# Kernel optimization log

Measured on AMD Instinct MI355X. Metric: run time of the kernel, lower is better.

## Reference

```python
import jax, jax.numpy as jnp
import numpy as np

N_NODES = 50000
N_EDGES = 640000
HID = 128
EDGE_FEAT = 4
NUM_G = 20
R_MIN, R_MAX = 0.0, 10.0

def setup_inputs() -> dict:
    key = jax.random.key(0)
    ks = jax.random.split(key, 16)
    s = lambda d: 1.0 / np.sqrt(d)
    return {
        'h': jax.random.normal(ks[0], (N_NODES, HID), jnp.float32),
        'x': jax.random.normal(ks[1], (N_NODES, 3), jnp.float32),
        'edge_index': jax.random.randint(ks[2], (2, N_EDGES), 0, N_NODES, dtype=jnp.int64),
        'mask_ligand': jnp.ones((N_NODES,), jnp.float32),
        'edge_attr': jax.random.normal(ks[3], (N_EDGES, EDGE_FEAT), jnp.float32),
        'We1': jax.random.normal(ks[4], (2*HID+EDGE_FEAT+NUM_G, HID), jnp.float32) * s(2*HID+EDGE_FEAT+NUM_G),
        'be1': jnp.zeros((HID,), jnp.float32),
        'We2': jax.random.normal(ks[5], (HID, HID), jnp.float32) * s(HID),
        'be2': jnp.zeros((HID,), jnp.float32),
        'Winf': jax.random.normal(ks[6], (HID, 1), jnp.float32) * s(HID),
        'binf': jnp.zeros((1,), jnp.float32),
        'Wx1': jax.random.normal(ks[7], (HID, HID), jnp.float32) * s(HID),
        'bx1': jnp.zeros((HID,), jnp.float32),
        'Wx2': jax.random.normal(ks[8], (HID, 1), jnp.float32) * 0.001 * s(HID),
        'Wn1': jax.random.normal(ks[9], (2*HID, HID), jnp.float32) * s(2*HID),
        'bn1': jnp.zeros((HID,), jnp.float32),
        'Wn2': jax.random.normal(ks[10], (HID, HID), jnp.float32) * s(HID),
        'bn2': jnp.zeros((HID,), jnp.float32),
    }

def reference(h, x, edge_index, mask_ligand, edge_attr,
              We1, be1, We2, be2, Winf, binf, Wx1, bx1, Wx2, Wn1, bn1, Wn2, bn2):
    n = h.shape[0]
    src, dst = edge_index[0], edge_index[1]
    hi, hj = h[dst], h[src]                      # [E, H] gathers
    rel_x = x[dst] - x[src]                      # [E, 3]
    d_sq = jnp.sum(rel_x**2, axis=-1, keepdims=True)  # [E, 1]
    d = jnp.sqrt(d_sq + 1e-8)
    # GaussianSmearing(r_min=0, r_max=10, num_gaussians=20)
    offset = jnp.linspace(R_MIN, R_MAX, NUM_G, dtype=h.dtype)
    coeff = -0.5 / (offset[1] - offset[0])**2
    d_feat = jnp.exp(coeff * (d - offset)**2)    # [E, 20]
    edge_feat = jnp.concatenate([d_feat, edge_attr], axis=-1)
    # edge MLP (2 layers, silu, act_last=True)
    z = jnp.concatenate([hi, hj, edge_feat], axis=-1)
    mij = jax.nn.silu(jax.nn.silu(z @ We1 + be1) @ We2 + be2)  # [E, H]
    eij = jax.nn.sigmoid(mij @ Winf + binf)      # [E, 1]
    mi = jax.ops.segment_sum(mij * eij, dst, num_segments=n)   # [N, H]
    # node MLP (2 layers, silu, no act on last)
    nz = jnp.concatenate([mi, h], axis=-1)
    h_out = h + (jax.nn.silu(nz @ Wn1 + bn1) @ Wn2 + bn2)
    # coordinate update
    xg = jnp.tanh(jax.nn.silu(mij @ Wx1 + bx1) @ Wx2)          # [E, 1]
    delta_x = jax.ops.segment_sum(rel_x / (d + 1.0) * xg, dst, num_segments=n)
    x_out = x + delta_x * mask_ligand[:, None]
    return h_out, x_out
```

## Files before the change

kernel.cpp:

```cpp
#include <hip/hip_runtime.h>
#include <math.h>

#define NN 50000
#define NE 640000
#define H 128
#define EPB 32
#define NPB 32
#define ZB 296
#define BB 136
#define KP1 288
#define NZB 264
#define NBPAD 50176
#define HISTB (NE / 256)
#define CONVB 464
#define ALLOCB (NBPAD / 256)
#define HCONVB 3125

typedef __attribute__((ext_vector_type(8))) unsigned short u16x8;
typedef __attribute__((ext_vector_type(8))) __bf16 bf16x8;
typedef __attribute__((ext_vector_type(2))) __bf16 bf16x2;
typedef __attribute__((ext_vector_type(4))) float f32x4;

__device__ __forceinline__ float frcp(float x) {
#if __has_builtin(__builtin_amdgcn_rcpf)
    return __builtin_amdgcn_rcpf(x);
#else
    return 1.0f / x;
#endif
}

__device__ __forceinline__ float silu_f(float v) {
    return v * frcp(1.0f + __expf(-v));
}

__device__ __forceinline__ float sigmoid_f(float v) {
    return frcp(1.0f + __expf(-v));
}

__device__ __forceinline__ float tanh_f(float v) {
    return 1.0f - 2.0f * frcp(1.0f + __expf(2.0f * v));
}

__device__ __forceinline__ unsigned short f2bf(float f) {
    unsigned int u = __builtin_bit_cast(unsigned int, f);
    u += 0x7FFFu + ((u >> 16) & 1u);
    return (unsigned short)(u >> 16);
}

__device__ __forceinline__ float bf2f(unsigned short s) {
    unsigned int u = ((unsigned int)s) << 16;
    return __builtin_bit_cast(float, u);
}

__device__ __forceinline__ unsigned int pkbf(float lo, float hi) {
#if __has_builtin(__builtin_amdgcn_cvt_pk_bf16_f32)
    bf16x2 v = __builtin_amdgcn_cvt_pk_bf16_f32(lo, hi);
    unsigned int r; __builtin_memcpy(&r, &v, 4); return r;
#else
    return (unsigned int)f2bf(lo) | ((unsigned int)f2bf(hi) << 16);
#endif
}

__device__ __forceinline__ f32x4 mfma16(u16x8 a, u16x8 b, f32x4 c) {
    return __builtin_amdgcn_mfma_f32_16x16x32_bf16(
        __builtin_bit_cast(bf16x8, a), __builtin_bit_cast(bf16x8, b), c, 0, 0, 0);
}

template<int KT, int INSTR, bool SYNC_BEFORE_EPI>
__device__ __forceinline__ void layer_mfma(
    const unsigned short* __restrict__ inbuf,
    const unsigned short* __restrict__ wt,
    const float* __restrict__ bias,
    unsigned short* __restrict__ outbuf,
    int wv, int quad, int r16)
{
    f32x4 acc[2][2] = {};
    const int F = wv * 32;
    #pragma unroll
    for (int ks = 0; ks < KT / 32; ks++) {
        int ko = ks * 32 + quad * 8;
        u16x8 b0 = *(const u16x8*)(inbuf + r16 * INSTR + ko);
        u16x8 b1 = *(const u16x8*)(inbuf + (16 + r16) * INSTR + ko);
        u16x8 a0 = *(const u16x8*)(wt + (size_t)(F + r16) * KT + ko);
        u16x8 a1 = *(const u16x8*)(wt + (size_t)(F + 16 + r16) * KT + ko);
        acc[0][0] = mfma16(a0, b0, acc[0][0]);
        acc[0][1] = mfma16(a0, b1, acc[0][1]);
        acc[1][0] = mfma16(a1, b0, acc[1][0]);
        acc[1][1] = mfma16(a1, b1, acc[1][1]);
    }
    if (SYNC_BEFORE_EPI) __syncthreads();
    #pragma unroll
    for (int rt = 0; rt < 2; rt++) {
        int f0 = F + rt * 16 + quad * 4;
        float4 bv = *(const float4*)(bias + f0);
        #pragma unroll
        for (int ci = 0; ci < 2; ci++) {
            int e = ci * 16 + r16;
            float s0 = silu_f(acc[rt][ci][0] + bv.x);
            float s1 = silu_f(acc[rt][ci][1] + bv.y);
            float s2 = silu_f(acc[rt][ci][2] + bv.z);
            float s3 = silu_f(acc[rt][ci][3] + bv.w);
            uint2 p = { pkbf(s0, s1), pkbf(s2, s3) };
            *(uint2*)(outbuf + e * BB + f0) = p;
        }
    }
}

__global__ __launch_bounds__(256) void init_kernel(
    float4* __restrict__ out4, int n4out,
    float4* __restrict__ ws4, int n4ws)
{
    int i = blockIdx.x * 256 + threadIdx.x;
    float4 z = make_float4(0.f, 0.f, 0.f, 0.f);
    if (i < n4out) out4[i] = z;
    else if (i - n4out < n4ws) ws4[i - n4out] = z;
}

__global__ __launch_bounds__(256) void hist_conv_kernel(
    const int* __restrict__ ei, int* __restrict__ cnt, int histBlocks,
    const float* __restrict__ We1, const float* __restrict__ We2,
    const float* __restrict__ Wx1, const float* __restrict__ Wn1,
    const float* __restrict__ Wn2,
    unsigned short* __restrict__ w1t, unsigned short* __restrict__ w2t,
    unsigned short* __restrict__ wx1t, unsigned short* __restrict__ wn1t,
    unsigned short* __restrict__ wn2t)
{
    int b = blockIdx.x, t = threadIdx.x;
    if (b < histBlocks) {
        int i = b * 256 + t;
        atomicAdd(&cnt[ei[NE + i]], 1);
        return;
    }
    int i = (b - histBlocks) * 256 + t;
    const int S1 = 128 * KP1;
    const int S2 = 128 * 128;
    const int S3 = 128 * 256;
    if (i < S1) {
        int n = i / KP1, k = i % KP1;
        w1t[i] = (k < 280) ? f2bf(We1[k * H + n]) : (unsigned short)0;
    } else if (i < S1 + S2) {
        int j = i - S1; int n = j / H, k = j % H;
        w2t[j] = f2bf(We2[k * H + n]);
    } else if (i < S1 + 2 * S2) {
        int j = i - S1 - S2; int n = j / H, k = j % H;
        wx1t[j] = f2bf(Wx1[k * H + n]);
    } else if (i < S1 + 2 * S2 + S3) {
        int j = i - S1 - 2 * S2; int n = j / 256, k = j % 256;
        wn1t[j] = f2bf(Wn1[k * H + n]);
    } else if (i < S1 + 3 * S2 + S3) {
        int j = i - S1 - 2 * S2 - S3; int n = j / H, k = j % H;
        wn2t[j] = f2bf(Wn2[k * H + n]);
    }
}

__global__ __launch_bounds__(256) void alloc_hconv_kernel(
    const int* __restrict__ cnt, int* __restrict__ cur, int* __restrict__ gtot,
    const float* __restrict__ h, unsigned short* __restrict__ hb,
    int allocBlocks)
{
    int b = blockIdx.x, t = threadIdx.x;
    if (b < allocBlocks) {
        int d = b * 256 + t;
        int v = cnt[d];
        int incl = v;
        #pragma unroll
        for (int o = 1; o < 64; o <<= 1) {
            int u = __shfl_up(incl, o, 64);
            if ((t & 63) >= o) incl += u;
        }
        int total = __shfl(incl, 63, 64);
        int base = 0;
        if ((t & 63) == 63) base = atomicAdd(gtot, total);
        base = __shfl(base, 63, 64);
        cur[d] = base + incl - v;
        return;
    }
    int j = (b - allocBlocks) * 256 + t;
    const float4* hp = (const float4*)h + (size_t)j * 2;
    float4 a = hp[0], c = hp[1];
    uint4 pk = { pkbf(a.x, a.y), pkbf(a.z, a.w), pkbf(c.x, c.y), pkbf(c.z, c.w) };
    ((uint4*)hb)[j] = pk;
}

__global__ __launch_bounds__(256) void scatter_kernel(
    const int* __restrict__ ei, const float* __restrict__ edge_attr,
    int* __restrict__ cur, uint4* __restrict__ epay)
{
    int i = blockIdx.x * 256 + threadIdx.x;
    int s = ei[i], d = ei[NE + i];
    float4 ea = ((const float4*)edge_attr)[i];
    int p = atomicAdd(&cur[d], 1);
    uint4 pv = { (unsigned)s, (unsigned)d, pkbf(ea.x, ea.y), pkbf(ea.z, ea.w) };
    epay[p] = pv;
}

__global__ __launch_bounds__(256, 7) void edge_kernel(
    const float* __restrict__ h, const float* __restrict__ x,
    const int* __restrict__ ei, const float* __restrict__ edge_attr,
    const unsigned short* __restrict__ w1t, const float* __restrict__ be1,
    const unsigned short* __restrict__ w2t, const float* __restrict__ be2,
    const float* __restrict__ Winf, const float* __restrict__ binf,
    const unsigned short* __restrict__ wx1t, const float* __restrict__ bx1,
    const float* __restrict__ Wx2,
    const uint4* __restrict__ epay, const unsigned short* __restrict__ hb,
    float* __restrict__ mi, float* __restrict__ dx)
{
    __shared__ unsigned short zs[EPB * ZB];
    __shared__ float relx_s[EPB][3];
    __shared__ float eij_s[EPB];
    __shared__ float epart[4][EPB];
    __shared__ float xpart[4][EPB];
    __shared__ int dst_s[EPB];
    __shared__ float winf_s[H];
    __shared__ float wx2_s[H];

    unsigned short* m1 = zs;
    unsigned short* m2 = zs + EPB * BB;

    const int t = threadIdx.x;
    const int e0 = blockIdx.x * EPB;
    const bool srt = (epay != nullptr);

    if (t >= 128 && t < 256) {
        winf_s[t - 128] = Winf[t - 128];
        wx2_s[t - 128] = Wx2[t - 128];
    }

    {
        int e = t >> 3, l = t & 7;
        unsigned short* zr = zs + e * ZB;
        if (srt) {
            uint4 pv = epay[e0 + e];
            const uint4* hd = (const uint4*)(hb + (size_t)pv.y * H);
            const uint4* hs = (const uint4*)(hb + (size_t)pv.x * H);
            uint4 a0 = hd[l * 2], a1 = hd[l * 2 + 1];
            *(uint4*)(zr + l * 16) = a0;
            *(uint4*)(zr + l * 16 + 8) = a1;
            uint4 c0 = hs[l * 2], c1 = hs[l * 2 + 1];
            *(uint4*)(zr + 128 + l * 16) = c0;
            *(uint4*)(zr + 128 + l * 16 + 8) = c1;
        } else {
            int s = ei[e0 + e], d = ei[NE + e0 + e];
            const float4* hd = (const float4*)(h + (size_t)d * H);
            const float4* hs = (const float4*)(h + (size_t)s * H);
            float4 v0 = hd[l * 4 + 0], v1 = hd[l * 4 + 1];
            float4 v2 = hd[l * 4 + 2], v3 = hd[l * 4 + 3];
            uint4 p0 = { pkbf(v0.x, v0.y), pkbf(v0.z, v0.w), pkbf(v1.x, v1.y), pkbf(v1.z, v1.w) };
            uint4 p1 = { pkbf(v2.x, v2.y), pkbf(v2.z, v2.w), pkbf(v3.x, v3.y), pkbf(v3.z, v3.w) };
            *(uint4*)(zr + l * 16) = p0;
            *(uint4*)(zr + l * 16 + 8) = p1;
            float4 w0 = hs[l * 4 + 0], w1 = hs[l * 4 + 1];
            float4 w2 = hs[l * 4 + 2], w3 = hs[l * 4 + 3];
            uint4 q0 = { pkbf(w0.x, w0.y), pkbf(w0.z, w0.w), pkbf(w1.x, w1.y), pkbf(w1.z, w1.w) };
            uint4 q1 = { pkbf(w2.x, w2.y), pkbf(w2.z, w2.w), pkbf(w3.x, w3.y), pkbf(w3.z, w3.w) };
            *(uint4*)(zr + 128 + l * 16) = q0;
            *(uint4*)(zr + 128 + l * 16 + 8) = q1;
        }
    }
    if (t < EPB) {
        unsigned short* zr = zs + t * ZB;
        int s, d;
        if (srt) {
            uint4 pv = epay[e0 + t];
            s = (int)pv.x; d = (int)pv.y;
            *(unsigned int*)(zr + 276) = pv.z;
            *(unsigned int*)(zr + 278) = pv.w;
        } else {
            s = ei[e0 + t]; d = ei[NE + e0 + t];
            #pragma unroll
            for (int j = 0; j < 4; j++)
                zr[276 + j] = f2bf(edge_attr[(size_t)(e0 + t) * 4 + j]);
        }
        dst_s[t] = d;
        float rx = x[d * 3 + 0] - x[s * 3 + 0];
        float ry = x[d * 3 + 1] - x[s * 3 + 1];
        float rz = x[d * 3 + 2] - x[s * 3 + 2];
        float d2 = rx * rx + ry * ry + rz * rz;
        float dd = sqrtf(d2 + 1e-8f);
        float inv = frcp(dd + 1.0f);
        relx_s[t][0] = rx * inv;
        relx_s[t][1] = ry * inv;
        relx_s[t][2] = rz * inv;
        const float step = 10.0f / 19.0f;
        const float coeff = -0.5f / (step * step);
        #pragma unroll
        for (int g = 0; g < 20; g++) {
            float df = dd - step * (float)g;
            zr[256 + g] = f2bf(__expf(coeff * df * df));
        }
        #pragma unroll
        for (int j = 280; j < ZB; j++) zr[j] = 0;
    }
    __syncthreads();

    const int wv = t >> 6, lane = t & 63;
    const int quad = lane >> 4, r16 = lane & 15;
    const int F = wv * 32;

    layer_mfma<KP1, ZB, true>(zs, w1t, be1, m1, wv, quad, r16);
    __syncthreads();

    {
        f32x4 acc[2][2] = {};
        #pragma unroll
        for (int ks = 0; ks < H / 32; ks++) {
            int ko = ks * 32 + quad * 8;
            u16x8 b0 = *(const u16x8*)(m1 + r16 * BB + ko);
            u16x8 b1 = *(const u16x8*)(m1 + (16 + r16) * BB + ko);
            u16x8 a0 = *(const u16x8*)(w2t + (size_t)(F + r16) * H + ko);
            u16x8 a1 = *(const u16x8*)(w2t + (size_t)(F + 16 + r16) * H + ko);
            acc[0][0] = mfma16(a0, b0, acc[0][0]);
            acc[0][1] = mfma16(a0, b1, acc[0][1]);
            acc[1][0] = mfma16(a1, b0, acc[1][0]);
            acc[1][1] = mfma16(a1, b1, acc[1][1]);
        }
        float ep[2] = {0.f, 0.f};
        #pragma unroll
        for (int rt = 0; rt < 2; rt++) {
            int f0 = F + rt * 16 + quad * 4;
            float4 bv = *(const float4*)(be2 + f0);
            float4 wf = *(const float4*)(winf_s + f0);
            #pragma unroll
            for (int ci = 0; ci < 2; ci++) {
                int e = ci * 16 + r16;
                float s0 = silu_f(acc[rt][ci][0] + bv.x);
                float s1 = silu_f(acc[rt][ci][1] + bv.y);
                float s2 = silu_f(acc[rt][ci][2] + bv.z);
                float s3 = silu_f(acc[rt][ci][3] + bv.w);
                ep[ci] += s0 * wf.x + s1 * wf.y + s2 * wf.z + s3 * wf.w;
                uint2 p = { pkbf(s0, s1), pkbf(s2, s3) };
                *(uint2*)(m2 + e * BB + f0) = p;
            }
        }
        #pragma unroll
        for (int ci = 0; ci < 2; ci++) {
            ep[ci] += __shfl_xor(ep[ci], 16, 64);
            ep[ci] += __shfl_xor(ep[ci], 32, 64);
        }
        if (quad == 0) {
            epart[wv][r16] = ep[0];
            epart[wv][16 + r16] = ep[1];
        }
    }
    __syncthreads();

    if (t < EPB) {
        float s = epart[0][t] + epart[1][t] + epart[2][t] + epart[3][t] + binf[0];
        eij_s[t] = sigmoid_f(s);
    }

    {
        f32x4 acc[2][2] = {};
        #pragma unroll
        for (int ks = 0; ks < H / 32; ks++) {
            int ko = ks * 32 + quad * 8;
            u16x8 b0 = *(const u16x8*)(m2 + r16 * BB + ko);
            u16x8 b1 = *(const u16x8*)(m2 + (16 + r16) * BB + ko);
            u16x8 a0 = *(const u16x8*)(wx1t + (size_t)(F + r16) * H + ko);
            u16x8 a1 = *(const u16x8*)(wx1t + (size_t)(F + 16 + r16) * H + ko);
            acc[0][0] = mfma16(a0, b0, acc[0][0]);
            acc[0][1] = mfma16(a0, b1, acc[0][1]);
            acc[1][0] = mfma16(a1, b0, acc[1][0]);
            acc[1][1] = mfma16(a1, b1, acc[1][1]);
        }
        float xp[2] = {0.f, 0.f};
        #pragma unroll
        for (int rt = 0; rt < 2; rt++) {
            int f0 = F + rt * 16 + quad * 4;
            float4 bv = *(const float4*)(bx1 + f0);
            float4 wf = *(const float4*)(wx2_s + f0);
            #pragma unroll
            for (int ci = 0; ci < 2; ci++) {
                xp[ci] += silu_f(acc[rt][ci][0] + bv.x) * wf.x
                        + silu_f(acc[rt][ci][1] + bv.y) * wf.y
                        + silu_f(acc[rt][ci][2] + bv.z) * wf.z
                        + silu_f(acc[rt][ci][3] + bv.w) * wf.w;
            }
        }
        #pragma unroll
        for (int ci = 0; ci < 2; ci++) {
            xp[ci] += __shfl_xor(xp[ci], 16, 64);
            xp[ci] += __shfl_xor(xp[ci], 32, 64);
        }
        if (quad == 0) {
            xpart[wv][r16] = xp[0];
            xpart[wv][16 + r16] = xp[1];
        }
    }
    __syncthreads();

    {
        if (t < 128) {
            const int k = t;
            float acc = 0.f;
            int rs = 0;
            #pragma unroll 1
            for (int e = 0; e < EPB; e++) {
                acc += bf2f(m2[e * BB + k]) * eij_s[e];
                if (e == EPB - 1 || dst_s[e + 1] != dst_s[e]) {
                    float* p = &mi[(size_t)dst_s[e] * H + k];
                    if (srt && rs > 0 && e < EPB - 1) *p = acc;
                    else atomicAdd(p, acc);
                    acc = 0.f;
                    rs = e + 1;
                }
            }
        } else if (t < 131) {
            const int dd = t - 128;
            float acc = 0.f;
            #pragma unroll 1
            for (int e = 0; e < EPB; e++) {
                float xs = xpart[0][e] + xpart[1][e] + xpart[2][e] + xpart[3][e];
                acc += relx_s[e][dd] * tanh_f(xs);
                if (e == EPB - 1 || dst_s[e + 1] != dst_s[e]) {
                    atomicAdd(&dx[(size_t)dst_s[e] * 3 + dd], acc);
                    acc = 0.f;
                }
            }
        }
    }
}

__global__ __launch_bounds__(256, 8) void node_kernel(
    const float* __restrict__ h, const float* __restrict__ x,
    const float* __restrict__ mask,
    const unsigned short* __restrict__ wn1t, const float* __restrict__ bn1,
    const unsigned short* __restrict__ wn2t, const float* __restrict__ bn2,
    float* __restrict__ mi_hout, float* __restrict__ dx_xout)
{
    __shared__ unsigned short nzs[NPB * NZB];

    unsigned short* nbuf = nzs;

    const int t = threadIdx.x;
    const int n0 = blockIdx.x * NPB;

    {
        int r = t >> 3, l = t & 7;
        int n = n0 + r;
        unsigned short* zr = nzs + r * NZB;
        if (n < NN) {
            const float4* mi4 = (const float4*)(mi_hout + (size_t)n * H);
            const float4* h4  = (const float4*)(h + (size_t)n * H);
            float4 v0 = mi4[l * 4 + 0], v1 = mi4[l * 4 + 1];
            float4 v2 = mi4[l * 4 + 2], v3 = mi4[l * 4 + 3];
            uint4 p0 = { pkbf(v0.x, v0.y), pkbf(v0.z, v0.w), pkbf(v1.x, v1.y), pkbf(v1.z, v1.w) };
            uint4 p1 = { pkbf(v2.x, v2.y), pkbf(v2.z, v2.w), pkbf(v3.x, v3.y), pkbf(v3.z, v3.w) };
            *(uint4*)(zr + l * 16) = p0;
            *(uint4*)(zr + l * 16 + 8) = p1;
            float4 w0 = h4[l * 4 + 0], w1 = h4[l * 4 + 1];
            float4 w2 = h4[l * 4 + 2], w3 = h4[l * 4 + 3];
            uint4 q0 = { pkbf(w0.x, w0.y), pkbf(w0.z, w0.w), pkbf(w1.x, w1.y), pkbf(w1.z, w1.w) };
            uint4 q1 = { pkbf(w2.x, w2.y), pkbf(w2.z, w2.w), pkbf(w3.x, w3.y), pkbf(w3.z, w3.w) };
            *(uint4*)(zr + 128 + l * 16) = q0;
            *(uint4*)(zr + 128 + l * 16 + 8) = q1;
        } else {
            uint4 zf = {0u, 0u, 0u, 0u};
            *(uint4*)(zr + l * 16) = zf;
            *(uint4*)(zr + l * 16 + 8) = zf;
            *(uint4*)(zr + 128 + l * 16) = zf;
            *(uint4*)(zr + 128 + l * 16 + 8) = zf;
        }
    }

    float xo = 0.f;
    int xn = -1, xdim = 0;
    if (t < NPB * 3) {
        int r = t / 3; xdim = t % 3;
        int n = n0 + r;
        if (n < NN) {
            xn = n;
            xo = x[(size_t)n * 3 + xdim] + dx_xout[(size_t)n * 3 + xdim] * mask[n];
        }
    }
    __syncthreads();

    if (xn >= 0) dx_xout[(size_t)xn * 3 + xdim] = xo;

    const int wv = t >> 6, lane = t & 63;
    const int quad = lane >> 4, r16 = lane & 15;

    layer_mfma<2 * H, NZB, true>(nzs, wn1t, bn1, nbuf, wv, quad, r16);
    __syncthreads();

    {
        f32x4 acc[2][2] = {};
        const int F = wv * 32;
        #pragma unroll
        for (int ks = 0; ks < H / 32; ks++) {
            int ko = ks * 32 + quad * 8;
            u16x8 b0 = *(const u16x8*)(nbuf + r16 * BB + ko);
            u16x8 b1 = *(const u16x8*)(nbuf + (16 + r16) * BB + ko);
            u16x8 a0 = *(const u16x8*)(wn2t + (size_t)(F + r16) * H + ko);
            u16x8 a1 = *(const u16x8*)(wn2t + (size_t)(F + 16 + r16) * H + ko);
            acc[0][0] = mfma16(a0, b0, acc[0][0]);
            acc[0][1] = mfma16(a0, b1, acc[0][1]);
            acc[1][0] = mfma16(a1, b0, acc[1][0]);
            acc[1][1] = mfma16(a1, b1, acc[1][1]);
        }
        #pragma unroll
        for (int rt = 0; rt < 2; rt++) {
            int f0 = F + rt * 16 + quad * 4;
            float4 bv = *(const float4*)(bn2 + f0);
            #pragma unroll
            for (int ci = 0; ci < 2; ci++) {
                int n = n0 + ci * 16 + r16;
                if (n < NN) {
                    float4 hv = *(const float4*)(h + (size_t)n * H + f0);
                    float4 o;
                    o.x = hv.x + acc[rt][ci][0] + bv.x;
                    o.y = hv.y + acc[rt][ci][1] + bv.y;
                    o.z = hv.z + acc[rt][ci][2] + bv.z;
                    o.w = hv.w + acc[rt][ci][3] + bv.w;
                    *(float4*)(mi_hout + (size_t)n * H + f0) = o;
                }
            }
        }
    }
}

extern "C" void kernel_launch(void* const* d_in, const int* in_sizes, int n_in,
                              void* d_out, int out_size, void* d_ws, size_t ws_size,
                              hipStream_t stream) {
    const float* h     = (const float*)d_in[0];
    const float* x     = (const float*)d_in[1];
    const int*   ei    = (const int*)d_in[2];
    const float* mask  = (const float*)d_in[3];
    const float* eattr = (const float*)d_in[4];
    const float* We1   = (const float*)d_in[5];
    const float* be1   = (const float*)d_in[6];
    const float* We2   = (const float*)d_in[7];
    const float* be2   = (const float*)d_in[8];
    const float* Winf  = (const float*)d_in[9];
    const float* binf  = (const float*)d_in[10];
    const float* Wx1   = (const float*)d_in[11];
    const float* bx1   = (const float*)d_in[12];
    const float* Wx2   = (const float*)d_in[13];
    const float* Wn1   = (const float*)d_in[14];
    const float* bn1   = (const float*)d_in[15];
    const float* Wn2   = (const float*)d_in[16];
    const float* bn2   = (const float*)d_in[17];

    float* mi = (float*)d_out;
    float* dx = mi + (size_t)NN * H;

    char* wsb  = (char*)d_ws;
    unsigned short* w1t  = (unsigned short*)wsb;
    unsigned short* w2t  = w1t + 128 * KP1;
    unsigned short* wx1t = w2t + 128 * H;
    unsigned short* wn1t = wx1t + 128 * H;
    unsigned short* wn2t = wn1t + 128 * 256;

    const size_t OFF_CNT  = 262144;
    const size_t OFF_CUR  = OFF_CNT + (size_t)NBPAD * 4;
    const size_t OFF_GTOT = OFF_CUR + (size_t)NBPAD * 4;
    const size_t OFF_HB   = OFF_GTOT + 16;
    const size_t OFF_EPAY = OFF_HB + (size_t)NN * H * 2;
    const size_t WS_NEED  = OFF_EPAY + (size_t)NE * 16;

    int*   cnt  = (int*)(wsb + OFF_CNT);
    int*   cur  = (int*)(wsb + OFF_CUR);
    int*   gtot = (int*)(wsb + OFF_GTOT);
    unsigned short* hb = (unsigned short*)(wsb + OFF_HB);
    uint4* epay = (uint4*)(wsb + OFF_EPAY);

    const bool full = (ws_size >= WS_NEED);

    const int n4out = (NN * H + NN * 3) / 4;
    const int n4ws  = full ? (int)((OFF_HB - OFF_CNT) / 16) : 0;
    init_kernel<<<(n4out + n4ws + 255) / 256, 256, 0, stream>>>(
        (float4*)d_out, n4out, (float4*)(wsb + OFF_CNT), n4ws);

    {
        int hb_ = full ? HISTB : 0;
        hist_conv_kernel<<<hb_ + CONVB, 256, 0, stream>>>(
            ei, cnt, hb_, We1, We2, Wx1, Wn1, Wn2, w1t, w2t, wx1t, wn1t, wn2t);
    }

    if (full) {
        alloc_hconv_kernel<<<ALLOCB + HCONVB, 256, 0, stream>>>(
            cnt, cur, gtot, h, hb, ALLOCB);
        scatter_kernel<<<NE / 256, 256, 0, stream>>>(ei, eattr, cur, epay);
    }

    edge_kernel<<<NE / EPB, 256, 0, stream>>>(
        h, x, ei, eattr, w1t, be1, w2t, be2, Winf, binf, wx1t, bx1, Wx2,
        full ? epay : (const uint4*)nullptr,
        full ? hb : (const unsigned short*)nullptr,
        mi, dx);

    node_kernel<<<(NN + NPB - 1) / NPB, 256, 0, stream>>>(
        h, x, mask, wn1t, bn1, wn2t, bn2, mi, dx);
}
```

Before: 511.7 us.

## Double edge tile to 64 edges with 512-thread blocks and reuse weight fragments

```diff
diff --git a/kernel.cpp b/kernel.cpp
--- a/kernel.cpp
+++ b/kernel.cpp
@@ -4,7 +4,7 @@
 #define NN 50000
 #define NE 640000
 #define H 128
-#define EPB 32
+#define EPB 64
 #define NPB 32
 #define ZB 296
 #define BB 136
@@ -194,7 +194,7 @@
     epay[p] = pv;
 }
 
-__global__ __launch_bounds__(256, 7) void edge_kernel(
+__global__ __launch_bounds__(512, 6) void edge_kernel(
     const float* __restrict__ h, const float* __restrict__ x,
     const int* __restrict__ ei, const float* __restrict__ edge_attr,
     const unsigned short* __restrict__ w1t, const float* __restrict__ be1,
@@ -208,8 +208,9 @@
     __shared__ unsigned short zs[EPB * ZB];
     __shared__ float relx_s[EPB][3];
     __shared__ float eij_s[EPB];
-    __shared__ float epart[4][EPB];
-    __shared__ float xpart[4][EPB];
+    __shared__ float xg_s[EPB];
+    __shared__ float epart[8][EPB];
+    __shared__ float xpart[8][EPB];
     __shared__ int dst_s[EPB];
     __shared__ float winf_s[H];
     __shared__ float wx2_s[H];
@@ -295,108 +296,139 @@
 
     const int wv = t >> 6, lane = t & 63;
     const int quad = lane >> 4, r16 = lane & 15;
-    const int F = wv * 32;
-
-    layer_mfma<KP1, ZB, true>(zs, w1t, be1, m1, wv, quad, r16);
+    const int F = wv * 16;
+    const int f0 = F + quad * 4;
+
+    {
+        f32x4 acc[4] = {};
+        #pragma unroll
+        for (int ks = 0; ks < KP1 / 32; ks++) {
+            int ko = ks * 32 + quad * 8;
+            u16x8 a = *(const u16x8*)(w1t + (size_t)(F + r16) * KP1 + ko);
+            #pragma unroll
+            for (int ci = 0; ci < 4; ci++) {
+                u16x8 b = *(const u16x8*)(zs + (ci * 16 + r16) * ZB + ko);
+                acc[ci] = mfma16(a, b, acc[ci]);
+            }
+        }
+        __syncthreads();
+        float4 bv = *(const float4*)(be1 + f0);
+        #pragma unroll
+        for (int ci = 0; ci < 4; ci++) {
+            int e = ci * 16 + r16;
+            float s0 = silu_f(acc[ci][0] + bv.x);
+            float s1 = silu_f(acc[ci][1] + bv.y);
+            float s2 = silu_f(acc[ci][2] + bv.z);
+            float s3 = silu_f(acc[ci][3] + bv.w);
+            uint2 p = { pkbf(s0, s1), pkbf(s2, s3) };
+            *(uint2*)(m1 + e * BB + f0) = p;
+        }
+    }
     __syncthreads();
 
     {
-        f32x4 acc[2][2] = {};
+        f32x4 acc[4] = {};
         #pragma unroll
         for (int ks = 0; ks < H / 32; ks++) {
             int ko = ks * 32 + quad * 8;
-            u16x8 b0 = *(const u16x8*)(m1 + r16 * BB + ko);
-            u16x8 b1 = *(const u16x8*)(m1 + (16 + r16) * BB + ko);
-            u16x8 a0 = *(const u16x8*)(w2t + (size_t)(F + r16) * H + ko);
-            u16x8 a1 = *(const u16x8*)(w2t + (size_t)(F + 16 + r16) * H + ko);
-            acc[0][0] = mfma16(a0, b0, acc[0][0]);
-            acc[0][1] = mfma16(a0, b1, acc[0][1]);
-            acc[1][0] = mfma16(a1, b0, acc[1][0]);
-            acc[1][1] = mfma16(a1, b1, acc[1][1]);
-        }
-        float ep[2] = {0.f, 0.f};
-        #pragma unroll
-        for (int rt = 0; rt < 2; rt++) {
-            int f0 = F + rt * 16 + quad * 4;
-            float4 bv = *(const float4*)(be2 + f0);
-            float4 wf = *(const float4*)(winf_s + f0);
-            #pragma unroll
-            for (int ci = 0; ci < 2; ci++) {
-                int e = ci * 16 + r16;
-                float s0 = silu_f(acc[rt][ci][0] + bv.x);
-                float s1 = silu_f(acc[rt][ci][1] + bv.y);
-                float s2 = silu_f(acc[rt][ci][2] + bv.z);
-                float s3 = silu_f(acc[rt][ci][3] + bv.w);
-                ep[ci] += s0 * wf.x + s1 * wf.y + s2 * wf.z + s3 * wf.w;
-                uint2 p = { pkbf(s0, s1), pkbf(s2, s3) };
-                *(uint2*)(m2 + e * BB + f0) = p;
+            u16x8 a = *(const u16x8*)(w2t + (size_t)(F + r16) * H + ko);
+            #pragma unroll
+            for (int ci = 0; ci < 4; ci++) {
+                u16x8 b = *(const u16x8*)(m1 + (ci * 16 + r16) * BB + ko);
+                acc[ci] = mfma16(a, b, acc[ci]);
             }
         }
-        #pragma unroll
-        for (int ci = 0; ci < 2; ci++) {
+        float4 bv = *(const float4*)(be2 + f0);
+        float4 wf = *(const float4*)(winf_s + f0);
+        float ep[4];
+        #pragma unroll
+        for (int ci = 0; ci < 4; ci++) {
+            int e = ci * 16 + r16;
+            float s0 = silu_f(acc[ci][0] + bv.x);
+            float s1 = silu_f(acc[ci][1] + bv.y);
+            float s2 = silu_f(acc[ci][2] + bv.z);
+            float s3 = silu_f(acc[ci][3] + bv.w);
+            ep[ci] = s0 * wf.x + s1 * wf.y + s2 * wf.z + s3 * wf.w;
+            uint2 p = { pkbf(s0, s1), pkbf(s2, s3) };
+            *(uint2*)(m2 + e * BB + f0) = p;
+        }
+        #pragma unroll
+        for (int ci = 0; ci < 4; ci++) {
             ep[ci] += __shfl_xor(ep[ci], 16, 64);
             ep[ci] += __shfl_xor(ep[ci], 32, 64);
         }
         if (quad == 0) {
-            epart[wv][r16] = ep[0];
-            epart[wv][16 + r16] = ep[1];
+            #pragma unroll
+            for (int ci = 0; ci < 4; ci++)
+                epart[wv][ci * 16 + r16] = ep[ci];
         }
     }
     __syncthreads();
 
     if (t < EPB) {
-        float s = epart[0][t] + epart[1][t] + epart[2][t] + epart[3][t] + binf[0];
+        float s = binf[0];
+        #pragma unroll
+        for (int w = 0; w < 8; w++) s += epart[w][t];
         eij_s[t] = sigmoid_f(s);
     }
 
     {
-        f32x4 acc[2][2] = {};
+        f32x4 acc[4] = {};
         #pragma unroll
         for (int ks = 0; ks < H / 32; ks++) {
             int ko = ks * 32 + quad * 8;
-            u16x8 b0 = *(const u16x8*)(m2 + r16 * BB + ko);
-            u16x8 b1 = *(const u16x8*)(m2 + (16 + r16) * BB + ko);
-            u16x8 a0 = *(const u16x8*)(wx1t + (size_t)(F + r16) * H + ko);
-            u16x8 a1 = *(const u16x8*)(wx1t + (size_t)(F + 16 + r16) * H + ko);
-            acc[0][0] = mfma16(a0, b0, acc[0][0]);
-            acc[0][1] = mfma16(a0, b1, acc[0][1]);
-            acc[1][0] = mfma16(a1, b0, acc[1][0]);
-            acc[1][1] = mfma16(a1, b1, acc[1][1]);
-        }
-        float xp[2] = {0.f, 0.f};
-        #pragma unroll
-        for (int rt = 0; rt < 2; rt++) {
-            int f0 = F + rt * 16 + quad * 4;
-            float4 bv = *(const float4*)(bx1 + f0);
-            float4 wf = *(const float4*)(wx2_s + f0);
-            #pragma unroll
-            for (int ci = 0; ci < 2; ci++) {
-                xp[ci] += silu_f(acc[rt][ci][0] + bv.x) * wf.x
-                        + silu_f(acc[rt][ci][1] + bv.y) * wf.y
-                        + silu_f(acc[rt][ci][2] + bv.z) * wf.z
-                        + silu_f(acc[rt][ci][3] + bv.w) * wf.w;
+            u16x8 a = *(const u16x8*)(wx1t + (size_t)(F + r16) * H + ko);
+            #pragma unroll
+            for (int ci = 0; ci < 4; ci++) {
+                u16x8 b = *(const u16x8*)(m2 + (ci * 16 + r16) * BB + ko);
+                acc[ci] = mfma16(a, b, acc[ci]);
             }
         }
-        #pragma unroll
-        for (int ci = 0; ci < 2; ci++) {
+        float4 bv = *(const float4*)(bx1 + f0);
+        float4 wf = *(const float4*)(wx2_s + f0);
+        float xp[4];
+        #pragma unroll
+        for (int ci = 0; ci < 4; ci++) {
+            xp[ci] = silu_f(acc[ci][0] + bv.x) * wf.x
+                   + silu_f(acc[ci][1] + bv.y) * wf.y
+                   + silu_f(acc[ci][2] + bv.z) * wf.z
+                   + silu_f(acc[ci][3] + bv.w) * wf.w;
+        }
+        #pragma unroll
+        for (int ci = 0; ci < 4; ci++) {
             xp[ci] += __shfl_xor(xp[ci], 16, 64);
             xp[ci] += __shfl_xor(xp[ci], 32, 64);
         }
         if (quad == 0) {
-            xpart[wv][r16] = xp[0];
-            xpart[wv][16 + r16] = xp[1];
+            #pragma unroll
+            for (int ci = 0; ci < 4; ci++)
+                xpart[wv][ci * 16 + r16] = xp[ci];
         }
     }
     __syncthreads();
 
-    {
-        if (t < 128) {
-            const int k = t;
-            float acc = 0.f;
-            int rs = 0;
-            #pragma unroll 1
-            for (int e = 0; e < EPB; e++) {
-                acc += bf2f(m2[e * BB + k]) * eij_s[e];
+    if (t < EPB) {
+        float xs = 0.f;
+        #pragma unroll
+        for (int w = 0; w < 8; w++) xs += xpart[w][t];
+        xg_s[t] = tanh_f(xs);
+    }
+    __syncthreads();
+
+    if (t < 128) {
+        const int k = t;
+        float acc = 0.f;
+        int rs = 0;
+        #pragma unroll
+        for (int c = 0; c < EPB; c += 8) {
+            float v[8];
+            #pragma unroll
+            for (int j = 0; j < 8; j++)
+                v[j] = bf2f(m2[(c + j) * BB + k]) * eij_s[c + j];
+            #pragma unroll
+            for (int j = 0; j < 8; j++) {
+                int e = c + j;
+                acc += v[j];
                 if (e == EPB - 1 || dst_s[e + 1] != dst_s[e]) {
                     float* p = &mi[(size_t)dst_s[e] * H + k];
                     if (srt && rs > 0 && e < EPB - 1) *p = acc;
@@ -405,16 +437,27 @@
                     rs = e + 1;
                 }
             }
-        } else if (t < 131) {
-            const int dd = t - 128;
-            float acc = 0.f;
-            #pragma unroll 1
-            for (int e = 0; e < EPB; e++) {
-                float xs = xpart[0][e] + xpart[1][e] + xpart[2][e] + xpart[3][e];
-                acc += relx_s[e][dd] * tanh_f(xs);
+        }
+    } else if (t < 131) {
+        const int dd = t - 128;
+        float acc = 0.f;
+        int rs = 0;
+        #pragma unroll
+        for (int c = 0; c < EPB; c += 8) {
+            float v[8];
+            #pragma unroll
+            for (int j = 0; j < 8; j++)
+                v[j] = relx_s[c + j][dd] * xg_s[c + j];
+            #pragma unroll
+            for (int j = 0; j < 8; j++) {
+                int e = c + j;
+                acc += v[j];
                 if (e == EPB - 1 || dst_s[e + 1] != dst_s[e]) {
-                    atomicAdd(&dx[(size_t)dst_s[e] * 3 + dd], acc);
+                    float* p = &dx[(size_t)dst_s[e] * 3 + dd];
+                    if (srt && rs > 0 && e < EPB - 1) *p = acc;
+                    else atomicAdd(p, acc);
                     acc = 0.f;
+                    rs = e + 1;
                 }
             }
         }
@@ -583,7 +626,7 @@
         scatter_kernel<<<NE / 256, 256, 0, stream>>>(ei, eattr, cur, epay);
     }
 
-    edge_kernel<<<NE / EPB, 256, 0, stream>>>(
+    edge_kernel<<<NE / EPB, 512, 0, stream>>>(
         h, x, ei, eattr, w1t, be1, w2t, be2, Winf, binf, wx1t, bx1, Wx2,
         full ? epay : (const uint4*)nullptr,
         full ? hb : (const unsigned short*)nullptr,
```

Measured after the change: 433.8 us. -15.2%, faster.
